# Kernel tuning notes

Hardware: AMD Instinct MI355X
Metric: run time of the kernel (lower is better)

The kernel has to match this reference:

```python
import jax, jax.numpy as jnp
import numpy as np

B, C, K, D = 256, 1000, 2, 128


def setup_inputs() -> dict:
    key = jax.random.key(0)
    k1, k2, k3 = jax.random.split(key, 3)
    z = jax.random.normal(k1, (B, D), dtype=jnp.float32)
    mu = jax.random.normal(k2, (C, K, D), dtype=jnp.float32) * 0.1
    logits_pi = jnp.zeros((C, K), dtype=jnp.float32)
    # identity Cholesky factors plus small strictly-lower noise (unit diagonal)
    noise = jnp.tril(jax.random.normal(k3, (C, K, D, D), dtype=jnp.float32), -1)
    covL = jnp.broadcast_to(jnp.eye(D, dtype=jnp.float32), (C, K, D, D)) + 0.01 * noise
    logits_prior = jnp.zeros((C,), dtype=jnp.float32)
    return {"z": z, "mu": mu, "logits_pi": logits_pi, "covL": covL, "logits_prior": logits_prior}


def reference(z, mu, logits_pi, covL, logits_prior):
    Bn, Dn = z.shape
    Cn, Kn = logits_pi.shape
    CK = Cn * Kn
    mu_f = mu.reshape(CK, Dn)               # (CK, D)
    L = covL.reshape(CK, Dn, Dn)            # (CK, D, D) lower triangular
    diff = z[None, :, :] - mu_f[:, None, :] # (CK, B, D)
    rhs = jnp.swapaxes(diff, 1, 2)          # (CK, D, B)
    y = jax.scipy.linalg.solve_triangular(L, rhs, lower=True)  # (CK, D, B)
    maha = jnp.sum(y * y, axis=1).T         # (B, CK)
    logdet = 2.0 * jnp.sum(jnp.log(jnp.diagonal(L, axis1=-2, axis2=-1)), axis=-1)  # (CK,)
    const = Dn * jnp.log(jnp.asarray(2.0 * jnp.pi, dtype=z.dtype))
    logpdf = (-0.5 * (maha + logdet[None, :] + const)).reshape(Bn, Cn, Kn)
    logpi = jax.nn.log_softmax(logits_pi, axis=-1)             # (C, K)
    log_pz_c = jax.scipy.special.logsumexp(logpdf + logpi[None], axis=-1)  # (B, C)
    return logits_prior[None, :] + log_pz_c
```

## Files before the change

kernel.cpp:

```cpp
#include <hip/hip_runtime.h>
#include <cstdint>

#define CC 1000
#define KK 2
#define DD 128

typedef short bf16x8 __attribute__((ext_vector_type(8)));
typedef float f32x16 __attribute__((ext_vector_type(16)));
typedef int   i32x4  __attribute__((ext_vector_type(4)));

__device__ __forceinline__ uint32_t f2bf(float f) {
    uint32_t x = __builtin_bit_cast(uint32_t, f);
    return (x + 0x7FFFu + ((x >> 16) & 1u)) >> 16;
}
__device__ __forceinline__ uint32_t pk2(float lo, float hi) {
    return f2bf(lo) | (f2bf(hi) << 16);
}
__device__ __forceinline__ f32x16 zero16() {
    f32x16 v;
    #pragma unroll
    for (int p = 0; p < 16; ++p) v[p] = 0.f;
    return v;
}

struct Frag8 { uint32_t a0, a1, a2, a3, b0, b1, b2, b3; };

__device__ __forceinline__ bf16x8 flo(const Frag8 f) {
    i32x4 t; t[0] = (int)f.a0; t[1] = (int)f.a1; t[2] = (int)f.a2; t[3] = (int)f.a3;
    return __builtin_bit_cast(bf16x8, t);
}
__device__ __forceinline__ bf16x8 fhi(const Frag8 f) {
    i32x4 t; t[0] = (int)f.b0; t[1] = (int)f.b1; t[2] = (int)f.b2; t[3] = (int)f.b3;
    return __builtin_bit_cast(bf16x8, t);
}

__device__ __forceinline__ Frag8 build_frags(const f32x16 t, int hp) {
    uint32_t W0 = pk2(t[0],  t[1]),  W1 = pk2(t[2],  t[3]);
    uint32_t W2 = pk2(t[4],  t[5]),  W3 = pk2(t[6],  t[7]);
    uint32_t W4 = pk2(t[8],  t[9]),  W5 = pk2(t[10], t[11]);
    uint32_t W6 = pk2(t[12], t[13]), W7 = pk2(t[14], t[15]);
    uint32_t s0 = (uint32_t)__shfl_xor((int)W0, 32, 64);
    uint32_t s1 = (uint32_t)__shfl_xor((int)W1, 32, 64);
    uint32_t s2 = (uint32_t)__shfl_xor((int)W2, 32, 64);
    uint32_t s3 = (uint32_t)__shfl_xor((int)W3, 32, 64);
    uint32_t s4 = (uint32_t)__shfl_xor((int)W4, 32, 64);
    uint32_t s5 = (uint32_t)__shfl_xor((int)W5, 32, 64);
    uint32_t s6 = (uint32_t)__shfl_xor((int)W6, 32, 64);
    uint32_t s7 = (uint32_t)__shfl_xor((int)W7, 32, 64);
    Frag8 f;
    f.a0 = hp ? s2 : W0;  f.a1 = hp ? s3 : W1;
    f.a2 = hp ? W2 : s0;  f.a3 = hp ? W3 : s1;
    f.b0 = hp ? s6 : W4;  f.b1 = hp ? s7 : W5;
    f.b2 = hp ? W6 : s4;  f.b3 = hp ? W7 : s5;
    return f;
}

__device__ __forceinline__ f32x16 off_apply(const char* Ep, const Frag8 yj, f32x16 acc) {
    bf16x8 A0 = *(const bf16x8*)(Ep);
    bf16x8 A1 = *(const bf16x8*)(Ep + 32);
    acc = __builtin_amdgcn_mfma_f32_32x32x16_bf16(A0, flo(yj), acc, 0, 0, 0);
    acc = __builtin_amdgcn_mfma_f32_32x32x16_bf16(A1, fhi(yj), acc, 0, 0, 0);
    return acc;
}
__device__ __forceinline__ f32x16 m_solve(const char* Mp, const Frag8 tf) {
    bf16x8 MA0 = *(const bf16x8*)(Mp);
    bf16x8 MA1 = *(const bf16x8*)(Mp + 32);
    f32x16 y = zero16();
    y = __builtin_amdgcn_mfma_f32_32x32x16_bf16(MA0, flo(tf), y, 0, 0, 0);
    y = __builtin_amdgcn_mfma_f32_32x32x16_bf16(MA1, fhi(tf), y, 0, 0, 0);
    return y;
}

__global__ __launch_bounds__(256, 1) void mda_partial_kernel(
    const float* __restrict__ z,
    const float* __restrict__ mu,
    const float* __restrict__ covL,
    float* __restrict__ ws)
{
    __shared__ __align__(16) char E[35840];
    __shared__ float RD[DD];
    __shared__ float LG[2];

    const int bid = blockIdx.x;
    const int c   = bid >> 2;
    const int k   = (bid >> 1) & 1;
    const int h   = bid & 1;
    const int tid = threadIdx.x;
    const int w   = tid >> 6, l = tid & 63, l31 = l & 31, hp = l >> 5;
    const int bcol = h * 128 + w * 32 + l31;
    const float* zb = z + (size_t)bcol * DD;
    const int off = l31 * 80 + 16 * hp;

    const float* Lm  = covL + (int64_t)(c*KK + k) * (DD*DD);
    const float* muv = mu + (size_t)(c*KK + k) * DD;

    if (tid < DD) {
        float dg = Lm[(size_t)tid * DD + tid];
        RD[tid] = 1.0f / dg;
        float lg = __logf(dg);
        #pragma unroll
        for (int o = 32; o; o >>= 1) lg += __shfl_down(lg, o, 64);
        if (l == 0) LG[tid >> 6] = lg;
    }
    __syncthreads();
    const float sld = LG[0] + LG[1];

    {
        #pragma unroll
        for (int rep = 0; rep < 6; ++rep) {
            int t2 = tid + 256*rep;
            int blk = t2 >> 8, r = (t2 >> 3) & 31, c4 = t2 & 7;
            int ib = 1 + (blk >= 1) + (blk >= 3);
            int jb = blk - ((ib * (ib - 1)) >> 1);
            float4 v = *(const float4*)(Lm + (size_t)(32*ib + r)*DD + 32*jb + 4*c4);
            uint2 u; u.x = pk2(-v.x, -v.y); u.y = pk2(-v.z, -v.w);
            *(uint2*)(E + blk*2560 + r*80 + 8*c4) = u;
        }
        #pragma unroll
        for (int rep = 0; rep < 4; ++rep) {
            int t3 = tid + 256*rep;
            int ib = t3 >> 8, r = (t3 >> 3) & 31, c4 = t3 & 7;
            float4 v = *(const float4*)(Lm + (size_t)(32*ib + r)*DD + 32*ib + 4*c4);
            float rdr = RD[32*ib + r];
            int n0 = 4*c4;
            float se0 = (n0+0 < r) ? -v.x*rdr : 0.f;
            float se1 = (n0+1 < r) ? -v.y*rdr : 0.f;
            float se2 = (n0+2 < r) ? -v.z*rdr : 0.f;
            float se3 = (n0+3 < r) ? -v.w*rdr : 0.f;
            char* tt = E + 25600 + ib*2560 + 2*r;
            *(unsigned short*)(tt + (n0+0)*80) = (unsigned short)f2bf((n0+0 == r) ? 1.f : se0);
            *(unsigned short*)(tt + (n0+1)*80) = (unsigned short)f2bf((n0+1 == r) ? 1.f : se1);
            *(unsigned short*)(tt + (n0+2)*80) = (unsigned short)f2bf((n0+2 == r) ? 1.f : se2);
            *(unsigned short*)(tt + (n0+3)*80) = (unsigned short)f2bf((n0+3 == r) ? 1.f : se3);
            uint2 u; u.x = pk2(se0, se1); u.y = pk2(se2, se3);
            *(uint2*)(E + 15360 + ib*2560 + r*80 + 8*c4) = u;
        }
    }
    __syncthreads();

    {
        const char* SmB = E + 15360 + w*2560;
        const char* TtB = E + 25600 + w*2560;
        bf16x8 A0 = *(const bf16x8*)(SmB + l31*80 + 16*hp);
        bf16x8 A1 = *(const bf16x8*)(SmB + l31*80 + 32 + 16*hp);
        bf16x8 B0 = *(const bf16x8*)(TtB + l31*80 + 16*hp);
        bf16x8 B1 = *(const bf16x8*)(TtB + l31*80 + 32 + 16*hp);
        f32x16 mm = zero16();
        mm = __builtin_amdgcn_mfma_f32_32x32x16_bf16(A0, B0, mm, 0,0,0);
        mm = __builtin_amdgcn_mfma_f32_32x32x16_bf16(A1, B1, mm, 0,0,0);
        float rdn = RD[32*w + l31];
        char* SmW = E + 15360 + w*2560;
        #pragma unroll
        for (int p = 0; p < 16; ++p) {
            int rowp = (p&3) + 8*(p>>2) + 4*hp;
            float mval = (mm[p] + ((rowp == l31) ? 1.f : 0.f)) * rdn;
            *(unsigned short*)(SmW + rowp*80 + 2*l31) = (unsigned short)f2bf(mval);
        }
    }
    __syncthreads();

    float macc = 0.f;
    f32x16 acc, yv;
    Frag8 tf, y0, y1, y2;

    #define LOAD_R(i)                                                        \
        do {                                                                 \
            _Pragma("unroll")                                                \
            for (int q = 0; q < 4; ++q) {                                    \
                float4 zv = *(const float4*)(zb + 32*(i) + 8*q + 4*hp);      \
                float4 mv = *(const float4*)(muv + 32*(i) + 8*q + 4*hp);     \
                acc[4*q+0] = zv.x - mv.x;  acc[4*q+1] = zv.y - mv.y;         \
                acc[4*q+2] = zv.z - mv.z;  acc[4*q+3] = zv.w - mv.w;         \
            }                                                                \
        } while (0)
    #define SQACC()                                                          \
        do {                                                                 \
            _Pragma("unroll")                                                \
            for (int p = 0; p < 16; ++p) macc += yv[p] * yv[p];              \
        } while (0)

    LOAD_R(0);
    tf = build_frags(acc, hp);
    yv = m_solve(E + 15360 + 0*2560 + off, tf);
    SQACC();
    y0 = build_frags(yv, hp);
    LOAD_R(1);
    acc = off_apply(E + 0*2560 + off, y0, acc);
    tf = build_frags(acc, hp);
    yv = m_solve(E + 15360 + 1*2560 + off, tf);
    SQACC();
    y1 = build_frags(yv, hp);
    LOAD_R(2);
    acc = off_apply(E + 1*2560 + off, y0, acc);
    acc = off_apply(E + 2*2560 + off, y1, acc);
    tf = build_frags(acc, hp);
    yv = m_solve(E + 15360 + 2*2560 + off, tf);
    SQACC();
    y2 = build_frags(yv, hp);
    LOAD_R(3);
    acc = off_apply(E + 3*2560 + off, y0, acc);
    acc = off_apply(E + 4*2560 + off, y1, acc);
    acc = off_apply(E + 5*2560 + off, y2, acc);
    tf = build_frags(acc, hp);
    yv = m_solve(E + 15360 + 3*2560 + off, tf);
    SQACC();
    #undef LOAD_R
    #undef SQACC

    macc += __shfl_xor(macc, 32, 64);

    const float CST = 235.2482645f;
    float lp = -0.5f * (macc + 2.f * sld + CST);
    if (hp == 0) {
        ws[(size_t)k * (256 * CC) + (size_t)bcol * CC + c] = lp;
    }
}

__global__ __launch_bounds__(256) void mda_combine_kernel(
    const float* __restrict__ ws,
    const float* __restrict__ logits_pi,
    const float* __restrict__ prior,
    float* __restrict__ out)
{
    int idx = blockIdx.x * 256 + threadIdx.x;
    int c = idx % CC;
    float lp0 = ws[idx];
    float lp1 = ws[256 * CC + idx];
    float pi0 = logits_pi[c*2+0], pi1 = logits_pi[c*2+1];
    float mp = fmaxf(pi0, pi1);
    float lsepi = mp + __logf(__expf(pi0-mp) + __expf(pi1-mp));
    float t0 = lp0 + pi0, t1 = lp1 + pi1;
    float mt = fmaxf(t0, t1);
    out[idx] = prior[c] + mt + __logf(__expf(t0-mt) + __expf(t1-mt)) - lsepi;
}

extern "C" void kernel_launch(void* const* d_in, const int* in_sizes, int n_in,
                              void* d_out, int out_size, void* d_ws, size_t ws_size,
                              hipStream_t stream) {
    const float* z         = (const float*)d_in[0];
    const float* mu        = (const float*)d_in[1];
    const float* logits_pi = (const float*)d_in[2];
    const float* covL      = (const float*)d_in[3];
    const float* prior     = (const float*)d_in[4];
    float* out = (float*)d_out;
    float* ws  = (float*)d_ws;

    hipLaunchKernelGGL(mda_partial_kernel, dim3(4*CC), dim3(256), 0, stream,
                       z, mu, covL, ws);
    hipLaunchKernelGGL(mda_combine_kernel, dim3(256 * CC / 256), dim3(256), 0, stream,
                       ws, logits_pi, prior, out);
}
```

Baseline: 62.54 us.

## Split per-component triangular-factor prep into separate kernel and reuse across batch halves

Adds a prep kernel that reads each Cholesky factor once, computes log-diagonal, and builds bf16 packed off-diagonal blocks and inverted diagonal blocks into workspace in an MFMA-friendly layout. The solve kernel then just copies 20KB of prepped data into LDS and runs the blocked MFMA triangular solve. Previously each of the two batch-half blocks redid the prep. This removes that duplicated work at the cost of an extra launch and a 40MB workspace round trip. It falls back to the old path when the workspace is too small.

```diff
diff --git a/kernel.cpp b/kernel.cpp
--- a/kernel.cpp
+++ b/kernel.cpp
@@ -4,6 +4,11 @@
 #define CC 1000
 #define KK 2
 #define DD 128
+
+#define WSE_BYTES   (2000u * 20480u)
+#define WSSLD_OFF   WSE_BYTES
+#define WSLP_OFF    (WSE_BYTES + 8000u)
+#define WS_NEEDED   (WSLP_OFF + 2048000u)
 
 typedef short bf16x8 __attribute__((ext_vector_type(8)));
 typedef float f32x16 __attribute__((ext_vector_type(16)));
@@ -55,6 +60,21 @@
     return f;
 }
 
+__device__ __forceinline__ f32x16 off_apply2(const char* Ep, const Frag8 yj, f32x16 acc) {
+    bf16x8 A0 = *(const bf16x8*)(Ep);
+    bf16x8 A1 = *(const bf16x8*)(Ep + 1024);
+    acc = __builtin_amdgcn_mfma_f32_32x32x16_bf16(A0, flo(yj), acc, 0, 0, 0);
+    acc = __builtin_amdgcn_mfma_f32_32x32x16_bf16(A1, fhi(yj), acc, 0, 0, 0);
+    return acc;
+}
+__device__ __forceinline__ f32x16 m_solve2(const char* Mp, const Frag8 tf) {
+    bf16x8 MA0 = *(const bf16x8*)(Mp);
+    bf16x8 MA1 = *(const bf16x8*)(Mp + 1024);
+    f32x16 y = zero16();
+    y = __builtin_amdgcn_mfma_f32_32x32x16_bf16(MA0, flo(tf), y, 0, 0, 0);
+    y = __builtin_amdgcn_mfma_f32_32x32x16_bf16(MA1, fhi(tf), y, 0, 0, 0);
+    return y;
+}
 __device__ __forceinline__ f32x16 off_apply(const char* Ep, const Frag8 yj, f32x16 acc) {
     bf16x8 A0 = *(const bf16x8*)(Ep);
     bf16x8 A1 = *(const bf16x8*)(Ep + 32);
@@ -71,11 +91,186 @@
     return y;
 }
 
-__global__ __launch_bounds__(256, 1) void mda_partial_kernel(
+
+__global__ __launch_bounds__(256, 1) void mda_prep_kernel(
+    const float* __restrict__ covL,
+    char* __restrict__ wsE,
+    float* __restrict__ wsSld)
+{
+    __shared__ __align__(16) char E[20480];
+    __shared__ float RD[DD];
+    __shared__ float LG[2];
+
+    const int ck  = blockIdx.x;
+    const int tid = threadIdx.x;
+    const int w   = tid >> 6, l = tid & 63, l31 = l & 31, hp = l >> 5;
+    const float* Lm = covL + (int64_t)ck * (DD*DD);
+    char* outE = wsE + (size_t)ck * 20480;
+
+    if (tid < DD) {
+        float dg = Lm[(size_t)tid * DD + tid];
+        RD[tid] = 1.0f / dg;
+        float lg = __logf(dg);
+        #pragma unroll
+        for (int o = 32; o; o >>= 1) lg += __shfl_down(lg, o, 64);
+        if (l == 0) LG[tid >> 6] = lg;
+    }
+    __syncthreads();
+    if (tid == 0) wsSld[ck] = LG[0] + LG[1];
+
+    #pragma unroll
+    for (int rep = 0; rep < 6; ++rep) {
+        int t2 = tid + 256*rep;
+        int blk = t2 >> 8, r = (t2 >> 3) & 31, c4 = t2 & 7;
+        int ib = 1 + (blk >= 1) + (blk >= 3);
+        int jb = blk - ((ib * (ib - 1)) >> 1);
+        float4 v = *(const float4*)(Lm + (size_t)(32*ib + r)*DD + 32*jb + 4*c4);
+        uint2 u; u.x = pk2(-v.x, -v.y); u.y = pk2(-v.z, -v.w);
+        int off = blk*2048 + (c4 >> 2)*1024 + ((((c4 >> 1) & 1)*32 + r)*16) + (c4 & 1)*8;
+        *(uint2*)(outE + off) = u;
+    }
+
+    #pragma unroll
+    for (int rep = 0; rep < 4; ++rep) {
+        int t3 = tid + 256*rep;
+        int ib = t3 >> 8, r = (t3 >> 3) & 31, c4 = t3 & 7;
+        float4 v = *(const float4*)(Lm + (size_t)(32*ib + r)*DD + 32*ib + 4*c4);
+        float rdr = RD[32*ib + r];
+        int n0 = 4*c4;
+        float se0 = (n0+0 < r) ? -v.x*rdr : 0.f;
+        float se1 = (n0+1 < r) ? -v.y*rdr : 0.f;
+        float se2 = (n0+2 < r) ? -v.z*rdr : 0.f;
+        float se3 = (n0+3 < r) ? -v.w*rdr : 0.f;
+        char* tt = E + 10240 + ib*2560 + 2*r;
+        *(unsigned short*)(tt + (n0+0)*80) = (unsigned short)f2bf((n0+0 == r) ? 1.f : se0);
+        *(unsigned short*)(tt + (n0+1)*80) = (unsigned short)f2bf((n0+1 == r) ? 1.f : se1);
+        *(unsigned short*)(tt + (n0+2)*80) = (unsigned short)f2bf((n0+2 == r) ? 1.f : se2);
+        *(unsigned short*)(tt + (n0+3)*80) = (unsigned short)f2bf((n0+3 == r) ? 1.f : se3);
+        uint2 u; u.x = pk2(se0, se1); u.y = pk2(se2, se3);
+        *(uint2*)(E + ib*2560 + r*80 + 8*c4) = u;
+    }
+    __syncthreads();
+
+    {
+        const char* SmB = E + w*2560;
+        const char* TtB = E + 10240 + w*2560;
+        bf16x8 A0 = *(const bf16x8*)(SmB + l31*80 + 16*hp);
+        bf16x8 A1 = *(const bf16x8*)(SmB + l31*80 + 32 + 16*hp);
+        bf16x8 B0 = *(const bf16x8*)(TtB + l31*80 + 16*hp);
+        bf16x8 B1 = *(const bf16x8*)(TtB + l31*80 + 32 + 16*hp);
+        f32x16 mm = zero16();
+        mm = __builtin_amdgcn_mfma_f32_32x32x16_bf16(A0, B0, mm, 0,0,0);
+        mm = __builtin_amdgcn_mfma_f32_32x32x16_bf16(A1, B1, mm, 0,0,0);
+        float rdn = RD[32*w + l31];
+        char* SmW = E + w*2560;
+        #pragma unroll
+        for (int p = 0; p < 16; ++p) {
+            int rowp = (p&3) + 8*(p>>2) + 4*hp;
+            float mval = (mm[p] + ((rowp == l31) ? 1.f : 0.f)) * rdn;
+            *(unsigned short*)(SmW + rowp*80 + 2*l31) = (unsigned short)f2bf(mval);
+        }
+    }
+    __syncthreads();
+
+    #pragma unroll
+    for (int rep = 0; rep < 4; ++rep) {
+        int t3 = tid + 256*rep;
+        int ib = t3 >> 8, r = (t3 >> 3) & 31, c4 = t3 & 7;
+        uint2 u = *(const uint2*)(E + ib*2560 + r*80 + 8*c4);
+        int off = (6 + ib)*2048 + (c4 >> 2)*1024 + ((((c4 >> 1) & 1)*32 + r)*16) + (c4 & 1)*8;
+        *(uint2*)(outE + off) = u;
+    }
+}
+
+__global__ __launch_bounds__(256, 1) void mda_solve_kernel(
     const float* __restrict__ z,
     const float* __restrict__ mu,
-    const float* __restrict__ covL,
-    float* __restrict__ ws)
+    const char* __restrict__ wsE,
+    const float* __restrict__ wsSld,
+    float* __restrict__ wsLp)
+{
+    __shared__ __align__(16) char EF[20480];
+
+    const int bid = blockIdx.x;
+    const int ck  = bid >> 1;
+    const int h   = bid & 1;
+    const int c   = ck >> 1, k = ck & 1;
+    const int tid = threadIdx.x;
+    const int w   = tid >> 6, l = tid & 63, l31 = l & 31, hp = l >> 5;
+    const int bcol = h * 128 + w * 32 + l31;
+    const float* zb  = z + (size_t)bcol * DD;
+    const float* muv = mu + (size_t)ck * DD;
+    const float sld  = wsSld[ck];
+
+    const char* src = wsE + (size_t)ck * 20480;
+    #pragma unroll
+    for (int rep = 0; rep < 5; ++rep) {
+        int o16 = (tid + 256*rep) * 16;
+        *(uint4*)(EF + o16) = *(const uint4*)(src + o16);
+    }
+    __syncthreads();
+
+    const int off = (hp * 32 + l31) * 16;
+
+    float macc = 0.f;
+    f32x16 acc, yv;
+    Frag8 tf, y0, y1, y2;
+
+    #define LOAD_R(i)                                                        \
+        do {                                                                 \
+            _Pragma("unroll")                                                \
+            for (int q = 0; q < 4; ++q) {                                    \
+                float4 zv = *(const float4*)(zb + 32*(i) + 8*q + 4*hp);      \
+                float4 mv = *(const float4*)(muv + 32*(i) + 8*q + 4*hp);     \
+                acc[4*q+0] = zv.x - mv.x;  acc[4*q+1] = zv.y - mv.y;         \
+                acc[4*q+2] = zv.z - mv.z;  acc[4*q+3] = zv.w - mv.w;         \
+            }                                                                \
+        } while (0)
+    #define SQACC()                                                          \
+        do {                                                                 \
+            _Pragma("unroll")                                                \
+            for (int p = 0; p < 16; ++p) macc += yv[p] * yv[p];              \
+        } while (0)
+
+    LOAD_R(0);
+    tf = build_frags(acc, hp);
+    yv = m_solve2(EF + 6*2048 + off, tf);
+    SQACC();
+    y0 = build_frags(yv, hp);
+    LOAD_R(1);
+    acc = off_apply2(EF + 0*2048 + off, y0, acc);
+    tf = build_frags(acc, hp);
+    yv = m_solve2(EF + 7*2048 + off, tf);
+    SQACC();
+    y1 = build_frags(yv, hp);
+    LOAD_R(2);
+    acc = off_apply2(EF + 1*2048 + off, y0, acc);
+    acc = off_apply2(EF + 2*2048 + off, y1, acc);
+    tf = build_frags(acc, hp);
+    yv = m_solve2(EF + 8*2048 + off, tf);
+    SQACC();
+    y2 = build_frags(yv, hp);
+    LOAD_R(3);
+    acc = off_apply2(EF + 3*2048 + off, y0, acc);
+    acc = off_apply2(EF + 4*2048 + off, y1, acc);
+    acc = off_apply2(EF + 5*2048 + off, y2, acc);
+    tf = build_frags(acc, hp);
+    yv = m_solve2(EF + 9*2048 + off, tf);
+    SQACC();
+    #undef LOAD_R
+    #undef SQACC
+
+    macc += __shfl_xor(macc, 32, 64);
+
+    const float CST = 235.2482645f;
+    float lp = -0.5f * (macc + 2.f * sld + CST);
+    if (hp == 0)
+        wsLp[(size_t)k * (256 * CC) + (size_t)bcol * CC + c] = lp;
+}
+
+__global__ __launch_bounds__(256, 1) void mda_partial_kernel(
+    const float* __restrict__ z, const float* __restrict__ mu,
+    const float* __restrict__ covL, float* __restrict__ ws)
 {
     __shared__ __align__(16) char E[35840];
     __shared__ float RD[DD];
@@ -211,21 +406,20 @@
 
     const float CST = 235.2482645f;
     float lp = -0.5f * (macc + 2.f * sld + CST);
-    if (hp == 0) {
+    if (hp == 0)
         ws[(size_t)k * (256 * CC) + (size_t)bcol * CC + c] = lp;
-    }
 }
 
 __global__ __launch_bounds__(256) void mda_combine_kernel(
-    const float* __restrict__ ws,
+    const float* __restrict__ lp,
     const float* __restrict__ logits_pi,
     const float* __restrict__ prior,
     float* __restrict__ out)
 {
     int idx = blockIdx.x * 256 + threadIdx.x;
     int c = idx % CC;
-    float lp0 = ws[idx];
-    float lp1 = ws[256 * CC + idx];
+    float lp0 = lp[idx];
+    float lp1 = lp[256 * CC + idx];
     float pi0 = logits_pi[c*2+0], pi1 = logits_pi[c*2+1];
     float mp = fmaxf(pi0, pi1);
     float lsepi = mp + __logf(__expf(pi0-mp) + __expf(pi1-mp));
@@ -243,10 +437,23 @@
     const float* covL      = (const float*)d_in[3];
     const float* prior     = (const float*)d_in[4];
     float* out = (float*)d_out;
-    float* ws  = (float*)d_ws;
-
-    hipLaunchKernelGGL(mda_partial_kernel, dim3(4*CC), dim3(256), 0, stream,
-                       z, mu, covL, ws);
-    hipLaunchKernelGGL(mda_combine_kernel, dim3(256 * CC / 256), dim3(256), 0, stream,
-                       ws, logits_pi, prior, out);
-}
+    char*  ws  = (char*)d_ws;
+
+    if (ws_size >= (size_t)WS_NEEDED) {
+        char*  wsE   = ws;
+        float* wsSld = (float*)(ws + WSSLD_OFF);
+        float* wsLp  = (float*)(ws + WSLP_OFF);
+        hipLaunchKernelGGL(mda_prep_kernel, dim3(2*CC), dim3(256), 0, stream,
+                           covL, wsE, wsSld);
+        hipLaunchKernelGGL(mda_solve_kernel, dim3(4*CC), dim3(256), 0, stream,
+                           z, mu, wsE, wsSld, wsLp);
+        hipLaunchKernelGGL(mda_combine_kernel, dim3(256 * CC / 256), dim3(256), 0, stream,
+                           wsLp, logits_pi, prior, out);
+    } else {
+        float* wsLp = (float*)ws;
+        hipLaunchKernelGGL(mda_partial_kernel, dim3(4*CC), dim3(256), 0, stream,
+                           z, mu, covL, wsLp);
+        hipLaunchKernelGGL(mda_combine_kernel, dim3(256 * CC / 256), dim3(256), 0, stream,
+                           wsLp, logits_pi, prior, out);
+    }
+}
```

Result: slower. 75.44 us (+20.6%).
